# Kernel optimization log

Hardware: AMD Instinct MI355X
Metric: run time of the kernel (lower is better)

The kernel has to match this reference:

```python
import jax, jax.numpy as jnp
import numpy as np

EMB_DIM = 1024
N_EXPERTS = 8
TOP_K = 2
MOE_HIDDEN = 1024
NORM_TOPK = True


def setup_inputs() -> dict:
    key = jax.random.key(0)
    ks = jax.random.split(key, 7)
    s = 0.02
    return {
        "x": jax.random.normal(ks[0], (2, 2048, EMB_DIM), dtype=jnp.float32),
        "router_w": jax.random.normal(ks[1], (N_EXPERTS, EMB_DIM), dtype=jnp.float32) * s,
        "router_b": jnp.zeros((N_EXPERTS,), dtype=jnp.float32),
        "gate_up_w": jax.random.normal(ks[2], (N_EXPERTS, 2 * MOE_HIDDEN, EMB_DIM), dtype=jnp.float32) * s,
        "gate_up_b": jnp.zeros((N_EXPERTS, 2 * MOE_HIDDEN), dtype=jnp.float32),
        "down_w": jax.random.normal(ks[3], (N_EXPERTS, EMB_DIM, MOE_HIDDEN), dtype=jnp.float32) * s,
        "down_b": jnp.zeros((N_EXPERTS, EMB_DIM), dtype=jnp.float32),
    }


def _swiglu(h):
    # SwiGLUFFN: even columns gate, odd columns up
    gate = h[:, ::2]
    up = h[:, 1::2]
    return jnp.clip(gate, -7.0, 7.0) * jax.nn.sigmoid(1.702 * gate) * (jnp.clip(up, -7.0, 7.0) + 1.0)


def reference(x, router_w, router_b, gate_up_w, gate_up_b, down_w, down_b):
    B, S, D = x.shape
    h = x.reshape(B * S, D)  # [T, D]
    # Router: linear -> top-k -> (softmax over k)
    scores = h @ router_w.T + router_b  # [T, E]
    vals, idx = jax.lax.top_k(scores, TOP_K)  # [T, K]
    if NORM_TOPK:
        vals = jax.nn.softmax(vals, axis=-1)
    # Combine weights per (token, expert); zero for unselected experts, so
    # masked-dense compute below is mathematically identical to gather/scatter.
    cw = jnp.sum(jax.nn.one_hot(idx, N_EXPERTS, dtype=vals.dtype) * vals[..., None], axis=1)  # [T, E]
    out = jnp.zeros_like(h)
    for e in range(N_EXPERTS):  # fixed small expert count
        g = h @ gate_up_w[e].T + gate_up_b[e]  # [T, 2H]
        a = _swiglu(g)  # [T, H]
        oe = a @ down_w[e].T + down_b[e]  # [T, D]
        out = out + oe * cw[:, e:e + 1]
    return out.reshape(B, S, D)
```

## Files before the change

### kernel.cpp

```cpp
#include <hip/hip_runtime.h>
#include <hip/hip_bf16.h>

#define EMB 1024
#define NEXP 8
#define NH 1024
#define N_GU 2048
#define TOPK 2

#define BK 64
#define KTILES 16
#define BN 128

#define BMG 128
#define MAXTG 72
#define GRID_GU (MAXTG * 16)
#define CONV_BLKS 256

#define BMD 64
#define MAXTD 160
#define GRID_DN (MAXTD * 8)

typedef __attribute__((ext_vector_type(4))) float f32x4;
typedef __attribute__((ext_vector_type(8))) short s16x8;
typedef __attribute__((ext_vector_type(4))) short s16x4;

typedef __attribute__((address_space(3))) unsigned int lds_u32;
typedef __attribute__((address_space(1))) const unsigned int glb_u32;

__device__ __forceinline__ void gl_lds16(const void* g, void* l) {
  __builtin_amdgcn_global_load_lds((glb_u32*)g, (lds_u32*)l, 16, 0, 0);
}

__device__ __forceinline__ unsigned short f2bf(float f) {
  union { float f; unsigned int u; } a; a.f = f;
  unsigned int u = a.u;
  unsigned int r = (u + 0x7FFFu + ((u >> 16) & 1u)) >> 16;
  return (unsigned short)r;
}

__device__ __forceinline__ float b2f(unsigned short h) {
  union { unsigned int u; float f; } a;
  a.u = ((unsigned int)h) << 16;
  return a.f;
}

__device__ __forceinline__ int xcd_swz(int bid, int nwg) {
  int q = nwg >> 3, r = nwg & 7;
  int xcd = bid & 7, pos = bid >> 3;
  int base = (xcd < r) ? xcd * (q + 1) : r * (q + 1) + (xcd - r) * q;
  return base + pos;
}

__global__ void router_convx(const float* __restrict__ x, unsigned short* __restrict__ xb, int n4x,
                             const float* __restrict__ rw, const float* __restrict__ rb, int T,
                             int* __restrict__ tokE, float* __restrict__ tokW) {
  int nr = T / 4;
  if ((int)blockIdx.x < nr) {
    int gwid = blockIdx.x * 4 + (threadIdx.x >> 6);
    int lane = threadIdx.x & 63;
    if (gwid >= T) return;
    const float* h = x + (size_t)gwid * EMB;
    float hreg[16];
    #pragma unroll
    for (int i = 0; i < 16; ++i) hreg[i] = h[lane + 64 * i];
    float sc[NEXP];
    #pragma unroll
    for (int e = 0; e < NEXP; ++e) {
      const float* w = rw + e * EMB;
      float s = 0.f;
      #pragma unroll
      for (int i = 0; i < 16; ++i) s += hreg[i] * w[lane + 64 * i];
      #pragma unroll
      for (int off = 32; off > 0; off >>= 1) s += __shfl_xor(s, off);
      sc[e] = s + rb[e];
    }
    if (lane == 0) {
      int e0 = 0; float v0 = sc[0];
      #pragma unroll
      for (int e = 1; e < NEXP; ++e) if (sc[e] > v0) { v0 = sc[e]; e0 = e; }
      int e1 = -1; float v1 = -3.0e38f;
      #pragma unroll
      for (int e = 0; e < NEXP; ++e) { if (e == e0) continue; if (sc[e] > v1) { v1 = sc[e]; e1 = e; } }
      float ex = __expf(v1 - v0);
      float w0 = 1.f / (1.f + ex);
      float w1 = ex / (1.f + ex);
      tokE[gwid * 2] = e0; tokE[gwid * 2 + 1] = e1;
      tokW[gwid * 2] = w0; tokW[gwid * 2 + 1] = w1;
    }
  } else {
    int base = (blockIdx.x - nr) * blockDim.x + threadIdx.x;
    int stride = (gridDim.x - nr) * blockDim.x;
    for (int i = base; i < n4x; i += stride) {
      float4 v = ((const float4*)x)[i];
      s16x4 o;
      o[0] = (short)f2bf(v.x);
      o[1] = (short)f2bf(v.y);
      o[2] = (short)f2bf(v.z);
      o[3] = (short)f2bf(v.w);
      ((s16x4*)xb)[i] = o;
    }
  }
}

__global__ void meta_convw(const int* __restrict__ tokE, int A,
                           int* __restrict__ tmG, int* __restrict__ tmD,
                           int* __restrict__ rows, int* __restrict__ apos,
                           const float* __restrict__ guw, unsigned short* __restrict__ guwb, int n4g) {
  if (blockIdx.x > 0) {
    int base = (blockIdx.x - 1) * blockDim.x + threadIdx.x;
    int stride = (gridDim.x - 1) * blockDim.x;
    for (int i = base; i < n4g; i += stride) {
      float4 v = ((const float4*)guw)[i];
      s16x4 o;
      o[0] = (short)f2bf(v.x);
      o[1] = (short)f2bf(v.y);
      o[2] = (short)f2bf(v.z);
      o[3] = (short)f2bf(v.w);
      ((s16x4*)guwb)[i] = o;
    }
    return;
  }
  __shared__ int hist[NEXP];
  __shared__ int offs[NEXP];
  __shared__ int fill[NEXP];
  int t = threadIdx.x;
  if (t < NEXP) { hist[t] = 0; fill[t] = 0; }
  __syncthreads();
  for (int i = t; i < A; i += blockDim.x) atomicAdd(&hist[tokE[i]], 1);
  __syncthreads();
  if (t == 0) {
    int off = 0, ntg = 0, ntd = 0;
    for (int e = 0; e < NEXP; ++e) {
      offs[e] = off;
      int c = hist[e];
      int ng = (c + BMG - 1) / BMG;
      for (int k = 0; k < ng; ++k) {
        tmG[1 + ntg * 3 + 0] = e;
        tmG[1 + ntg * 3 + 1] = off + k * BMG;
        tmG[1 + ntg * 3 + 2] = off + c;
        ntg++;
      }
      int nd = (c + BMD - 1) / BMD;
      for (int k = 0; k < nd; ++k) {
        tmD[1 + ntd * 3 + 0] = e;
        tmD[1 + ntd * 3 + 1] = off + k * BMD;
        tmD[1 + ntd * 3 + 2] = off + c;
        ntd++;
      }
      off += c;
    }
    tmG[0] = ntg;
    tmD[0] = ntd;
  }
  __syncthreads();
  for (int i = t; i < A; i += blockDim.x) {
    int e = tokE[i];
    int p = offs[e] + atomicAdd(&fill[e], 1);
    rows[p] = i >> 1;
    apos[i] = p;
  }
}

__global__ __launch_bounds__(256, 4) void gemm_gate_up(
    const unsigned short* __restrict__ xb,
    const unsigned short* __restrict__ gub,
    const float* __restrict__ gu_bias,
    const int* __restrict__ rows,
    const int* __restrict__ tilemeta,
    unsigned short* __restrict__ hact,
    const float* __restrict__ dw, unsigned short* __restrict__ dwb, int n4d) {
  __shared__ __align__(16) short As[BMG * BK];
  __shared__ __align__(16) short Bs[BN * BK];
  if ((int)blockIdx.x >= GRID_GU) {
    int base = ((int)blockIdx.x - GRID_GU) * blockDim.x + threadIdx.x;
    int stride = CONV_BLKS * blockDim.x;
    for (int i = base; i < n4d; i += stride) {
      float4 v = ((const float4*)dw)[i];
      s16x4 o;
      o[0] = (short)f2bf(v.x);
      o[1] = (short)f2bf(v.y);
      o[2] = (short)f2bf(v.z);
      o[3] = (short)f2bf(v.w);
      ((s16x4*)dwb)[i] = o;
    }
    return;
  }
  int wg = xcd_swz(blockIdx.x, GRID_GU);
  int tileid = wg >> 4;
  int n0 = (wg & 15) * BN;
  int nt = tilemeta[0];
  if (tileid >= nt) return;
  int e    = tilemeta[1 + tileid * 3 + 0];
  int m0   = tilemeta[1 + tileid * 3 + 1];
  int mEnd = tilemeta[1 + tileid * 3 + 2];

  int t = threadIdx.x;
  int lane = t & 63;
  int wid = t >> 6;
  int wr = wid >> 1, wc = wid & 1;

  int srow = lane >> 3;
  int scol = (((lane & 7) ^ (srow & 7)) * 8);
  const unsigned short* ga[4];
  const unsigned short* gb[4];
  int dstoff[4];
  #pragma unroll
  for (int q = 0; q < 4; ++q) {
    int rt = wid * 32 + q * 8 + srow;
    int ai = m0 + rt; if (ai >= mEnd) ai = mEnd - 1;
    ga[q] = xb + (size_t)rows[ai] * EMB + scol;
    gb[q] = gub + ((size_t)e * N_GU + n0 + rt) * EMB + scol;
    dstoff[q] = (wid * 32 + q * 8) * BK;
  }

  int fr = lane & 15;
  int q8 = (lane >> 4) * 8;
  int rsw = (fr & 7) << 3;

  f32x4 acc[4][4];
  #pragma unroll
  for (int i = 0; i < 4; ++i)
    #pragma unroll
    for (int j = 0; j < 4; ++j) acc[i][j] = (f32x4){0.f, 0.f, 0.f, 0.f};

  for (int tk = 0; tk < KTILES; ++tk) {
    int k0 = tk * BK;
    __syncthreads();
    #pragma unroll
    for (int q = 0; q < 4; ++q) {
      gl_lds16(ga[q] + k0, &As[dstoff[q]]);
      gl_lds16(gb[q] + k0, &Bs[dstoff[q]]);
    }
    __syncthreads();
    #pragma unroll
    for (int kk = 0; kk < BK; kk += 32) {
      s16x8 a[4], b[4];
      #pragma unroll
      for (int i = 0; i < 4; ++i)
        a[i] = *(const s16x8*)(&As[(wr * 64 + i * 16 + fr) * BK + ((kk + q8) ^ rsw)]);
      #pragma unroll
      for (int j = 0; j < 4; ++j)
        b[j] = *(const s16x8*)(&Bs[(wc * 64 + j * 16 + fr) * BK + ((kk + q8) ^ rsw)]);
      #pragma unroll
      for (int i = 0; i < 4; ++i)
        #pragma unroll
        for (int j = 0; j < 4; ++j)
          acc[i][j] = __builtin_amdgcn_mfma_f32_16x16x32_bf16(a[i], b[j], acc[i][j], 0, 0, 0);
    }
  }

  const float* bias_e = gu_bias + (size_t)e * N_GU;
  int rbase = m0 + wr * 64 + ((lane >> 4) * 4);
  #pragma unroll
  for (int i = 0; i < 4; ++i) {
    #pragma unroll
    for (int j = 0; j < 4; ++j) {
      int n = n0 + wc * 64 + j * 16 + fr;
      float v[4], o[4];
      #pragma unroll
      for (int r = 0; r < 4; ++r) v[r] = acc[i][j][r] + bias_e[n];
      #pragma unroll
      for (int r = 0; r < 4; ++r) o[r] = __shfl_xor(v[r], 1);
      if ((lane & 1) == 0) {
        int outc = n >> 1;
        #pragma unroll
        for (int r = 0; r < 4; ++r) {
          int pos = rbase + i * 16 + r;
          if (pos < mEnd) {
            float g = v[r], u = o[r];
            float gc = fminf(fmaxf(g, -7.f), 7.f);
            float uc = fminf(fmaxf(u, -7.f), 7.f);
            float sig = 1.f / (1.f + __expf(-1.702f * g));
            float act = gc * sig * (uc + 1.f);
            hact[(size_t)pos * NH + outc] = f2bf(act);
          }
        }
      }
    }
  }
}

__global__ __launch_bounds__(256, 6) void gemm_down(
    const unsigned short* __restrict__ hact,
    const unsigned short* __restrict__ dwb,
    const int* __restrict__ tilemeta,
    unsigned short* __restrict__ y) {
  __shared__ __align__(16) short As[BMD * BK];
  __shared__ __align__(16) short Bs[BN * BK];
  int wg = xcd_swz(blockIdx.x, gridDim.x);
  int tileid = wg >> 3;
  int n0 = (wg & 7) * BN;
  int nt = tilemeta[0];
  if (tileid >= nt) return;
  int e    = tilemeta[1 + tileid * 3 + 0];
  int m0   = tilemeta[1 + tileid * 3 + 1];
  int mEnd = tilemeta[1 + tileid * 3 + 2];

  int t = threadIdx.x;
  int lane = t & 63;
  int wid = t >> 6;
  int wr = wid >> 1, wc = wid & 1;

  int srow = lane >> 3;
  int scol = (((lane & 7) ^ (srow & 7)) * 8);
  const unsigned short* ga[2];
  const unsigned short* gb[4];
  int dstA[2], dstB[4];
  #pragma unroll
  for (int q = 0; q < 2; ++q) {
    int rt = q * 32 + wid * 8 + srow;
    int ai = m0 + rt; if (ai >= mEnd) ai = mEnd - 1;
    ga[q] = hact + (size_t)ai * NH + scol;
    dstA[q] = (q * 32 + wid * 8) * BK;
  }
  #pragma unroll
  for (int q = 0; q < 4; ++q) {
    int rt = q * 32 + wid * 8 + srow;
    gb[q] = dwb + ((size_t)e * EMB + n0 + rt) * NH + scol;
    dstB[q] = (q * 32 + wid * 8) * BK;
  }

  int fr = lane & 15;
  int q8 = (lane >> 4) * 8;
  int rsw = (fr & 7) << 3;

  f32x4 acc[2][4];
  #pragma unroll
  for (int i = 0; i < 2; ++i)
    #pragma unroll
    for (int j = 0; j < 4; ++j) acc[i][j] = (f32x4){0.f, 0.f, 0.f, 0.f};

  for (int tk = 0; tk < KTILES; ++tk) {
    int k0 = tk * BK;
    __syncthreads();
    #pragma unroll
    for (int q = 0; q < 2; ++q) gl_lds16(ga[q] + k0, &As[dstA[q]]);
    #pragma unroll
    for (int q = 0; q < 4; ++q) gl_lds16(gb[q] + k0, &Bs[dstB[q]]);
    __syncthreads();
    #pragma unroll
    for (int kk = 0; kk < BK; kk += 32) {
      s16x8 a[2], b[4];
      #pragma unroll
      for (int i = 0; i < 2; ++i)
        a[i] = *(const s16x8*)(&As[(wr * 32 + i * 16 + fr) * BK + ((kk + q8) ^ rsw)]);
      #pragma unroll
      for (int j = 0; j < 4; ++j)
        b[j] = *(const s16x8*)(&Bs[(wc * 64 + j * 16 + fr) * BK + ((kk + q8) ^ rsw)]);
      #pragma unroll
      for (int i = 0; i < 2; ++i)
        #pragma unroll
        for (int j = 0; j < 4; ++j)
          acc[i][j] = __builtin_amdgcn_mfma_f32_16x16x32_bf16(a[i], b[j], acc[i][j], 0, 0, 0);
    }
  }

  int rbase = m0 + wr * 32 + ((lane >> 4) * 4);
  #pragma unroll
  for (int i = 0; i < 2; ++i) {
    #pragma unroll
    for (int j = 0; j < 4; ++j) {
      int n = n0 + wc * 64 + j * 16 + fr;
      #pragma unroll
      for (int r = 0; r < 4; ++r) {
        int pos = rbase + i * 16 + r;
        if (pos < mEnd) y[(size_t)pos * EMB + n] = f2bf(acc[i][j][r]);
      }
    }
  }
}

__global__ void combine_out(const unsigned short* __restrict__ y, const float* __restrict__ down_b,
                            const int* __restrict__ tokE, const float* __restrict__ tokW,
                            const int* __restrict__ apos, float* __restrict__ out, int T) {
  int i = blockIdx.x * blockDim.x + threadIdx.x;
  int tot = T * (EMB / 4);
  if (i >= tot) return;
  int tok = i >> 8;
  int c = i & 255;
  int e0 = tokE[tok * 2], e1 = tokE[tok * 2 + 1];
  float w0 = tokW[tok * 2], w1 = tokW[tok * 2 + 1];
  int p0 = apos[tok * 2], p1 = apos[tok * 2 + 1];
  s16x4 v0 = ((const s16x4*)(y + (size_t)p0 * EMB))[c];
  s16x4 v1 = ((const s16x4*)(y + (size_t)p1 * EMB))[c];
  float4 b0 = ((const float4*)(down_b + (size_t)e0 * EMB))[c];
  float4 b1 = ((const float4*)(down_b + (size_t)e1 * EMB))[c];
  float4 o;
  o.x = w0 * (b2f((unsigned short)v0[0]) + b0.x) + w1 * (b2f((unsigned short)v1[0]) + b1.x);
  o.y = w0 * (b2f((unsigned short)v0[1]) + b0.y) + w1 * (b2f((unsigned short)v1[1]) + b1.y);
  o.z = w0 * (b2f((unsigned short)v0[2]) + b0.z) + w1 * (b2f((unsigned short)v1[2]) + b1.z);
  o.w = w0 * (b2f((unsigned short)v0[3]) + b0.w) + w1 * (b2f((unsigned short)v1[3]) + b1.w);
  ((float4*)out)[i] = o;
}

extern "C" void kernel_launch(void* const* d_in, const int* in_sizes, int n_in,
                              void* d_out, int out_size, void* d_ws, size_t ws_size,
                              hipStream_t stream) {
  const float* x   = (const float*)d_in[0];
  const float* rw  = (const float*)d_in[1];
  const float* rb  = (const float*)d_in[2];
  const float* guw = (const float*)d_in[3];
  const float* gub = (const float*)d_in[4];
  const float* dw  = (const float*)d_in[5];
  const float* db  = (const float*)d_in[6];
  float* out = (float*)d_out;

  int T = in_sizes[0] / EMB;
  int A = T * TOPK;

  char* ws = (char*)d_ws;
  size_t off = 0;
  auto alloc = [&](size_t bytes) -> void* {
    void* p = ws + off;
    off = (off + bytes + 255) & ~((size_t)255);
    return p;
  };
  unsigned short* xb   = (unsigned short*)alloc((size_t)T * EMB * 2);
  unsigned short* guwb = (unsigned short*)alloc((size_t)NEXP * N_GU * EMB * 2);
  unsigned short* dwb  = (unsigned short*)alloc((size_t)NEXP * EMB * NH * 2);
  unsigned short* hact = (unsigned short*)alloc((size_t)A * NH * 2);
  unsigned short* y    = (unsigned short*)alloc((size_t)A * EMB * 2);
  int*   tokE    = (int*)alloc((size_t)A * 4);
  float* tokW    = (float*)alloc((size_t)A * 4);
  int*   apos    = (int*)alloc((size_t)A * 4);
  int*   rowsArr = (int*)alloc((size_t)A * 4);
  int*   tmG     = (int*)alloc((1 + MAXTG * 3) * 4);
  int*   tmD     = (int*)alloc((1 + MAXTD * 3) * 4);

  int n4x = T * EMB / 4;
  int n4g = NEXP * N_GU * EMB / 4;
  int n4d = NEXP * EMB * NH / 4;

  router_convx<<<T / 4 + 1024, 256, 0, stream>>>(x, xb, n4x, rw, rb, T, tokE, tokW);
  meta_convw<<<1 + 2048, 1024, 0, stream>>>(tokE, A, tmG, tmD, rowsArr, apos, guw, guwb, n4g);

  gemm_gate_up<<<GRID_GU + CONV_BLKS, 256, 0, stream>>>(xb, guwb, gub, rowsArr, tmG, hact,
                                                        dw, dwb, n4d);
  gemm_down<<<GRID_DN, 256, 0, stream>>>(hact, dwb, tmD, y);

  combine_out<<<(T * EMB / 4 + 255) / 256, 256, 0, stream>>>(y, db, tokE, tokW, apos, out, T);
}
```

Measured before the change: 133.4 us.

## Fuse fp32-to-bf16 weight conversion into GEMM tile loads, dropping separate conversion passes

Removes the standalone passes that converted gate_up and down weights to bf16 in workspace. Each GEMM instead loads fp32 weight rows into registers, packs them to bf16, and stores them swizzled into LDS. This avoids writing and rereading the bf16 weight copies. In exchange, the B operand no longer uses async global-to-LDS loads, each tile reads twice the bytes, and weights are reread per M tile in fp32.

```diff
diff --git a/kernel.cpp b/kernel.cpp
--- a/kernel.cpp
+++ b/kernel.cpp
@@ -14,7 +14,6 @@
 #define BMG 128
 #define MAXTG 72
 #define GRID_GU (MAXTG * 16)
-#define CONV_BLKS 256
 
 #define BMD 64
 #define MAXTD 160
@@ -42,6 +41,15 @@
   union { unsigned int u; float f; } a;
   a.u = ((unsigned int)h) << 16;
   return a.f;
+}
+
+__device__ __forceinline__ s16x8 pack8(float4 a, float4 b) {
+  s16x8 p;
+  p[0] = (short)f2bf(a.x); p[1] = (short)f2bf(a.y);
+  p[2] = (short)f2bf(a.z); p[3] = (short)f2bf(a.w);
+  p[4] = (short)f2bf(b.x); p[5] = (short)f2bf(b.y);
+  p[6] = (short)f2bf(b.z); p[7] = (short)f2bf(b.w);
+  return p;
 }
 
 __device__ __forceinline__ int xcd_swz(int bid, int nwg) {
@@ -102,24 +110,9 @@
   }
 }
 
-__global__ void meta_convw(const int* __restrict__ tokE, int A,
-                           int* __restrict__ tmG, int* __restrict__ tmD,
-                           int* __restrict__ rows, int* __restrict__ apos,
-                           const float* __restrict__ guw, unsigned short* __restrict__ guwb, int n4g) {
-  if (blockIdx.x > 0) {
-    int base = (blockIdx.x - 1) * blockDim.x + threadIdx.x;
-    int stride = (gridDim.x - 1) * blockDim.x;
-    for (int i = base; i < n4g; i += stride) {
-      float4 v = ((const float4*)guw)[i];
-      s16x4 o;
-      o[0] = (short)f2bf(v.x);
-      o[1] = (short)f2bf(v.y);
-      o[2] = (short)f2bf(v.z);
-      o[3] = (short)f2bf(v.w);
-      ((s16x4*)guwb)[i] = o;
-    }
-    return;
-  }
+__global__ void meta_scatter(const int* __restrict__ tokE, int A,
+                             int* __restrict__ tmG, int* __restrict__ tmD,
+                             int* __restrict__ rows, int* __restrict__ apos) {
   __shared__ int hist[NEXP];
   __shared__ int offs[NEXP];
   __shared__ int fill[NEXP];
@@ -163,28 +156,13 @@
 
 __global__ __launch_bounds__(256, 4) void gemm_gate_up(
     const unsigned short* __restrict__ xb,
-    const unsigned short* __restrict__ gub,
+    const float* __restrict__ guw,
     const float* __restrict__ gu_bias,
     const int* __restrict__ rows,
     const int* __restrict__ tilemeta,
-    unsigned short* __restrict__ hact,
-    const float* __restrict__ dw, unsigned short* __restrict__ dwb, int n4d) {
+    unsigned short* __restrict__ hact) {
   __shared__ __align__(16) short As[BMG * BK];
   __shared__ __align__(16) short Bs[BN * BK];
-  if ((int)blockIdx.x >= GRID_GU) {
-    int base = ((int)blockIdx.x - GRID_GU) * blockDim.x + threadIdx.x;
-    int stride = CONV_BLKS * blockDim.x;
-    for (int i = base; i < n4d; i += stride) {
-      float4 v = ((const float4*)dw)[i];
-      s16x4 o;
-      o[0] = (short)f2bf(v.x);
-      o[1] = (short)f2bf(v.y);
-      o[2] = (short)f2bf(v.z);
-      o[3] = (short)f2bf(v.w);
-      ((s16x4*)dwb)[i] = o;
-    }
-    return;
-  }
   int wg = xcd_swz(blockIdx.x, GRID_GU);
   int tileid = wg >> 4;
   int n0 = (wg & 15) * BN;
@@ -200,17 +178,19 @@
   int wr = wid >> 1, wc = wid & 1;
 
   int srow = lane >> 3;
-  int scol = (((lane & 7) ^ (srow & 7)) * 8);
+  int nchunk = lane & 7;
+  int scolA = ((nchunk ^ (srow & 7)) * 8);
   const unsigned short* ga[4];
-  const unsigned short* gb[4];
-  int dstoff[4];
+  const float* gbf[4];
+  int dstA[4], dstB[4];
   #pragma unroll
   for (int q = 0; q < 4; ++q) {
     int rt = wid * 32 + q * 8 + srow;
     int ai = m0 + rt; if (ai >= mEnd) ai = mEnd - 1;
-    ga[q] = xb + (size_t)rows[ai] * EMB + scol;
-    gb[q] = gub + ((size_t)e * N_GU + n0 + rt) * EMB + scol;
-    dstoff[q] = (wid * 32 + q * 8) * BK;
+    ga[q] = xb + (size_t)rows[ai] * EMB + scolA;
+    dstA[q] = (wid * 32 + q * 8) * BK;
+    gbf[q] = guw + ((size_t)e * N_GU + n0 + rt) * EMB + nchunk * 8;
+    dstB[q] = rt * BK + ((nchunk ^ (srow & 7)) * 8);
   }
 
   int fr = lane & 15;
@@ -227,10 +207,17 @@
     int k0 = tk * BK;
     __syncthreads();
     #pragma unroll
+    for (int q = 0; q < 4; ++q) gl_lds16(ga[q] + k0, &As[dstA[q]]);
+    float4 bl[4][2];
+    #pragma unroll
     for (int q = 0; q < 4; ++q) {
-      gl_lds16(ga[q] + k0, &As[dstoff[q]]);
-      gl_lds16(gb[q] + k0, &Bs[dstoff[q]]);
-    }
+      const float4* p = (const float4*)(gbf[q] + k0);
+      bl[q][0] = p[0];
+      bl[q][1] = p[1];
+    }
+    #pragma unroll
+    for (int q = 0; q < 4; ++q)
+      *(s16x8*)(&Bs[dstB[q]]) = pack8(bl[q][0], bl[q][1]);
     __syncthreads();
     #pragma unroll
     for (int kk = 0; kk < BK; kk += 32) {
@@ -282,7 +269,7 @@
 
 __global__ __launch_bounds__(256, 6) void gemm_down(
     const unsigned short* __restrict__ hact,
-    const unsigned short* __restrict__ dwb,
+    const float* __restrict__ dw,
     const int* __restrict__ tilemeta,
     unsigned short* __restrict__ y) {
   __shared__ __align__(16) short As[BMD * BK];
@@ -302,22 +289,23 @@
   int wr = wid >> 1, wc = wid & 1;
 
   int srow = lane >> 3;
-  int scol = (((lane & 7) ^ (srow & 7)) * 8);
+  int nchunk = lane & 7;
+  int scolA = ((nchunk ^ (srow & 7)) * 8);
   const unsigned short* ga[2];
-  const unsigned short* gb[4];
+  const float* gbf[4];
   int dstA[2], dstB[4];
   #pragma unroll
   for (int q = 0; q < 2; ++q) {
     int rt = q * 32 + wid * 8 + srow;
     int ai = m0 + rt; if (ai >= mEnd) ai = mEnd - 1;
-    ga[q] = hact + (size_t)ai * NH + scol;
+    ga[q] = hact + (size_t)ai * NH + scolA;
     dstA[q] = (q * 32 + wid * 8) * BK;
   }
   #pragma unroll
   for (int q = 0; q < 4; ++q) {
     int rt = q * 32 + wid * 8 + srow;
-    gb[q] = dwb + ((size_t)e * EMB + n0 + rt) * NH + scol;
-    dstB[q] = (q * 32 + wid * 8) * BK;
+    gbf[q] = dw + ((size_t)e * EMB + n0 + rt) * NH + nchunk * 8;
+    dstB[q] = rt * BK + ((nchunk ^ (srow & 7)) * 8);
   }
 
   int fr = lane & 15;
@@ -335,8 +323,16 @@
     __syncthreads();
     #pragma unroll
     for (int q = 0; q < 2; ++q) gl_lds16(ga[q] + k0, &As[dstA[q]]);
-    #pragma unroll
-    for (int q = 0; q < 4; ++q) gl_lds16(gb[q] + k0, &Bs[dstB[q]]);
+    float4 bl[4][2];
+    #pragma unroll
+    for (int q = 0; q < 4; ++q) {
+      const float4* p = (const float4*)(gbf[q] + k0);
+      bl[q][0] = p[0];
+      bl[q][1] = p[1];
+    }
+    #pragma unroll
+    for (int q = 0; q < 4; ++q)
+      *(s16x8*)(&Bs[dstB[q]]) = pack8(bl[q][0], bl[q][1]);
     __syncthreads();
     #pragma unroll
     for (int kk = 0; kk < BK; kk += 32) {
@@ -416,8 +412,6 @@
     return p;
   };
   unsigned short* xb   = (unsigned short*)alloc((size_t)T * EMB * 2);
-  unsigned short* guwb = (unsigned short*)alloc((size_t)NEXP * N_GU * EMB * 2);
-  unsigned short* dwb  = (unsigned short*)alloc((size_t)NEXP * EMB * NH * 2);
   unsigned short* hact = (unsigned short*)alloc((size_t)A * NH * 2);
   unsigned short* y    = (unsigned short*)alloc((size_t)A * EMB * 2);
   int*   tokE    = (int*)alloc((size_t)A * 4);
@@ -428,15 +422,12 @@
   int*   tmD     = (int*)alloc((1 + MAXTD * 3) * 4);
 
   int n4x = T * EMB / 4;
-  int n4g = NEXP * N_GU * EMB / 4;
-  int n4d = NEXP * EMB * NH / 4;
 
   router_convx<<<T / 4 + 1024, 256, 0, stream>>>(x, xb, n4x, rw, rb, T, tokE, tokW);
-  meta_convw<<<1 + 2048, 1024, 0, stream>>>(tokE, A, tmG, tmD, rowsArr, apos, guw, guwb, n4g);
-
-  gemm_gate_up<<<GRID_GU + CONV_BLKS, 256, 0, stream>>>(xb, guwb, gub, rowsArr, tmG, hact,
-                                                        dw, dwb, n4d);
-  gemm_down<<<GRID_DN, 256, 0, stream>>>(hact, dwb, tmD, y);
+  meta_scatter<<<1, 1024, 0, stream>>>(tokE, A, tmG, tmD, rowsArr, apos);
+
+  gemm_gate_up<<<GRID_GU, 256, 0, stream>>>(xb, guw, gub, rowsArr, tmG, hact);
+  gemm_down<<<GRID_DN, 256, 0, stream>>>(hact, dw, tmD, y);
 
   combine_out<<<(T * EMB / 4 + 255) / 256, 256, 0, stream>>>(y, db, tokE, tokW, apos, out, T);
 }
```

New measurement: 181.3 us. +36.0%, slower.
